# Kernel tuning notes

Measured on AMD Instinct MI355X. Metric: run time of the kernel, lower is better.

## Reference

```python
import jax, jax.numpy as jnp
import numpy as np

EPS = 1e-5

def _ln(x, g, b):
    mu = jnp.mean(x, axis=-1, keepdims=True)
    var = jnp.mean((x - mu) ** 2, axis=-1, keepdims=True)
    return (x - mu) * jax.lax.rsqrt(var + EPS) * g + b

def setup_inputs() -> dict:
    key = jax.random.key(0)
    ks = jax.random.split(key, 12)
    B, T, D, H = 8, 2048, 64, 8
    hs = D // H  # 8
    s = 0.05
    return {
        'x': jax.random.normal(ks[0], (B, T, D), dtype=jnp.float32),
        # per-head Q/K/V weights stacked: [H, hs, D] (torch Linear weight layout [out, in])
        'Wq': jax.random.normal(ks[1], (H, hs, D), dtype=jnp.float32) * s,
        'Wk': jax.random.normal(ks[2], (H, hs, D), dtype=jnp.float32) * s,
        'Wv': jax.random.normal(ks[3], (H, hs, D), dtype=jnp.float32) * s,
        'Wproj': jax.random.normal(ks[4], (D, H * hs), dtype=jnp.float32) * s,
        'bproj': jnp.zeros((D,), dtype=jnp.float32),
        'W1': jax.random.normal(ks[5], (4 * D, D), dtype=jnp.float32) * s,
        'b1': jnp.zeros((4 * D,), dtype=jnp.float32),
        'W2': jax.random.normal(ks[6], (D, 4 * D), dtype=jnp.float32) * s,
        'b2': jnp.zeros((D,), dtype=jnp.float32),
        'ln1_g': jnp.ones((D,), dtype=jnp.float32),
        'ln1_b': jnp.zeros((D,), dtype=jnp.float32),
        'ln2_g': jnp.ones((D,), dtype=jnp.float32),
        'ln2_b': jnp.zeros((D,), dtype=jnp.float32),
    }

def reference(x, Wq, Wk, Wv, Wproj, bproj, W1, b1, W2, b2, ln1_g, ln1_b, ln2_g, ln2_b):
    # pre-LN self-attention (dropout = identity, eval mode)
    h = _ln(x, ln1_g, ln1_b)
    q = jnp.einsum('btd,hsd->bhts', h, Wq)  # [B,H,T,hs]
    k = jnp.einsum('btd,hsd->bhts', h, Wk)
    v = jnp.einsum('btd,hsd->bhts', h, Wv)
    scale = Wk.shape[1] ** -0.5  # k.shape[-1]**-0.5 in original
    wei = jax.nn.softmax(jnp.einsum('bhts,bhus->bhtu', q, k) * scale, axis=-1)
    o = jnp.einsum('bhtu,bhus->bhts', wei, v)  # [B,H,T,hs]
    B, H, T, hs = o.shape
    o = o.transpose(0, 2, 1, 3).reshape(B, T, H * hs)  # concat heads
    x = x + o @ Wproj.T + bproj
    # pre-LN MLP
    h2 = _ln(x, ln2_g, ln2_b)
    ff = jax.nn.relu(h2 @ W1.T + b1) @ W2.T + b2
    return x + ff
```

## Files before the change

### kernel.cpp

```cpp
#include <hip/hip_runtime.h>
#include <hip/hip_fp16.h>

#define DEV static __device__ __forceinline__

constexpr int NTOK = 8 * 2048;
constexpr float LN_EPS = 1e-5f;

using half4  = __attribute__((ext_vector_type(4))) _Float16;
using half8  = __attribute__((ext_vector_type(8))) _Float16;
using f32x4  = __attribute__((ext_vector_type(4))) float;
using f32x16 = __attribute__((ext_vector_type(16))) float;

DEV __half2 bch2(unsigned u) { return __builtin_bit_cast(__half2, u); }
DEV unsigned bcu(__half2 h)  { return __builtin_bit_cast(unsigned, h); }

#define MFMA16(a, b, c)   __builtin_amdgcn_mfma_f32_16x16x16f16(a, b, c, 0, 0, 0)
#define MFMA32(a, b, c)   __builtin_amdgcn_mfma_f32_32x32x8f16(a, b, c, 0, 0, 0)
#define MFMA32X16(a, b, c) __builtin_amdgcn_mfma_f32_32x32x16_f16(a, b, c, 0, 0, 0)

DEV half4 pk4(float a, float b, float c, float d) {
  unsigned lo = __builtin_bit_cast(unsigned, __builtin_amdgcn_cvt_pkrtz(a, b));
  unsigned hi = __builtin_bit_cast(unsigned, __builtin_amdgcn_cvt_pkrtz(c, d));
  uint2 u = make_uint2(lo, hi);
  return __builtin_bit_cast(half4, u);
}
DEV half8 cat8(uint2 a, uint2 b) {
  uint4 u = make_uint4(a.x, a.y, b.x, b.y);
  return __builtin_bit_cast(half8, u);
}
DEV half8 cat8h(half4 a, half4 b) {
  return cat8(__builtin_bit_cast(uint2, a), __builtin_bit_cast(uint2, b));
}

DEV float schr(float x) {
  return __builtin_bit_cast(float, (int)__builtin_fmaf(x, 8388608.0f, 1064987473.0f));
}

__global__ __launch_bounds__(256) void k_ln_qkv(
    const float* __restrict__ x, const float* __restrict__ Wq,
    const float* __restrict__ Wk, const float* __restrict__ Wv,
    const float* __restrict__ g1, const float* __restrict__ b1g,
    __half* __restrict__ Qo, __half* __restrict__ Ko, __half* __restrict__ Vo)
{
  __shared__ __align__(16) __half WqF[4096];
  __shared__ __align__(16) __half WkF[4096];
  __shared__ __align__(16) __half WvF[4096];
  const int tid = threadIdx.x, lane = tid & 63, wid = tid >> 6;
  const int l15 = lane & 15, gg = lane >> 4;
  const float qs = 0.35355339059327373f * 1.4426950408889634f;
  for (int idx = tid; idx < 1024; idx += 256) {
    int mt = idx >> 8, kt = (idx >> 6) & 3, l = idx & 63;
    int row = l & 15, g = l >> 4;
    int off = (mt * 16 + row) * 64 + kt * 16 + g * 4;
    float4 a = *(const float4*)(Wq + off);
    float4 b = *(const float4*)(Wk + off);
    float4 c = *(const float4*)(Wv + off);
    half4 hq; hq[0] = (_Float16)(a.x*qs); hq[1] = (_Float16)(a.y*qs);
    hq[2] = (_Float16)(a.z*qs); hq[3] = (_Float16)(a.w*qs);
    half4 hk; hk[0] = (_Float16)b.x; hk[1] = (_Float16)b.y;
    hk[2] = (_Float16)b.z; hk[3] = (_Float16)b.w;
    half4 hv; hv[0] = (_Float16)c.x; hv[1] = (_Float16)c.y;
    hv[2] = (_Float16)c.z; hv[3] = (_Float16)c.w;
    *(half4*)&WqF[idx * 4] = hq;
    *(half4*)&WkF[idx * 4] = hk;
    *(half4*)&WvF[idx * 4] = hv;
  }
  __syncthreads();

  const int tok = (blockIdx.x * 4 + wid) * 16 + l15;
  const int b = tok >> 11, t = tok & 2047;
  float4 xv[4];
  float sum = 0.f, sq = 0.f;
  #pragma unroll
  for (int kt = 0; kt < 4; ++kt) {
    xv[kt] = *(const float4*)(x + tok * 64 + kt * 16 + gg * 4);
    sum += xv[kt].x + xv[kt].y + xv[kt].z + xv[kt].w;
    sq  += xv[kt].x*xv[kt].x + xv[kt].y*xv[kt].y
         + xv[kt].z*xv[kt].z + xv[kt].w*xv[kt].w;
  }
  sum += __shfl_xor(sum, 16); sum += __shfl_xor(sum, 32);
  sq  += __shfl_xor(sq, 16);  sq  += __shfl_xor(sq, 32);
  float mu = sum * (1.0f / 64.0f);
  float var = sq * (1.0f / 64.0f) - mu * mu;
  float rs = rsqrtf(var + LN_EPS);
  half4 hb[4];
  #pragma unroll
  for (int kt = 0; kt < 4; ++kt) {
    float4 gv = *(const float4*)(g1 + kt * 16 + gg * 4);
    float4 bv = *(const float4*)(b1g + kt * 16 + gg * 4);
    hb[kt][0] = (_Float16)((xv[kt].x - mu) * rs * gv.x + bv.x);
    hb[kt][1] = (_Float16)((xv[kt].y - mu) * rs * gv.y + bv.y);
    hb[kt][2] = (_Float16)((xv[kt].z - mu) * rs * gv.z + bv.z);
    hb[kt][3] = (_Float16)((xv[kt].w - mu) * rs * gv.w + bv.w);
  }
  const int sbase = gg * 4;
  #pragma unroll
  for (int mt = 0; mt < 4; ++mt) {
    f32x4 oq = {}, ok = {}, ov = {};
    #pragma unroll
    for (int kt = 0; kt < 4; ++kt) {
      half4 q_a = *(const half4*)&WqF[((mt * 4 + kt) * 64 + lane) * 4];
      half4 k_a = *(const half4*)&WkF[((mt * 4 + kt) * 64 + lane) * 4];
      half4 v_a = *(const half4*)&WvF[((mt * 4 + kt) * 64 + lane) * 4];
      oq = MFMA16(q_a, hb[kt], oq);
      ok = MFMA16(k_a, hb[kt], ok);
      ov = MFMA16(v_a, hb[kt], ov);
    }
    const int sg = mt * 16 + sbase;
    const int h = sg >> 3, s = sg & 7;
    const long base = ((long)(b * 8 + h) * 2048 + t) * 8 + s;
    *(half4*)(Qo + base) = pk4(oq[0], oq[1], oq[2], oq[3]);
    *(half4*)(Ko + base) = pk4(ok[0], ok[1], ok[2], ok[3]);
    *(half4*)(Vo + base) = pk4(ov[0], ov[1], ov[2], ov[3]);
  }
}

__global__ __launch_bounds__(256, 4) void k_attn(
    const __half* __restrict__ Qg, const __half* __restrict__ Kg,
    const __half* __restrict__ Vg, __half* __restrict__ Og)
{
  __shared__ __align__(16) char VTs[9 * 4128];
  const int tid = threadIdx.x, lane = tid & 63, wid = tid >> 6;
  const int bh = blockIdx.x;
  const int base = bh << 14;
  const uint4* Vu = (const uint4*)(Vg + base);
  for (int i = tid; i < 1024; i += 256) {
    uint4 a = Vu[2 * i], bq = Vu[2 * i + 1];
    const unsigned short* pa = (const unsigned short*)&a;
    const unsigned short* pb = (const unsigned short*)&bq;
    #pragma unroll
    for (int d = 0; d < 8; ++d) {
      unsigned val = (unsigned)pa[d] | ((unsigned)pb[d] << 16);
      *(unsigned*)(VTs + d * 4128 + i * 4) = val;
    }
    *(unsigned*)(VTs + 8 * 4128 + i * 4) = 0x3C003C00u;
  }
  __syncthreads();

  const int b = bh >> 3, hh = bh & 7;
  const int l31 = lane & 31, hi = lane >> 5;
  const int q0 = blockIdx.y * 128 + wid * 32;
  half4 qf = *(const half4*)((const char*)(Qg + base) + (q0 + l31) * 16 + hi * 8);
  const char* kp = (const char*)(Kg + base) + l31 * 16 + hi * 8;
  const int deff = (l31 <= 8) ? l31 : 8;
  const char* vb = VTs + deff * 4128 + hi * 8;

  const f32x16 z = {};
  f32x16 o0 = {};
  half4 kA[8], kB[8];
  #pragma unroll
  for (int u = 0; u < 8; ++u) kA[u] = *(const half4*)(kp + u * 512);

  #define ATTN_BODY(KF, VB, IMM)                                               \
    {                                                                          \
      f32x16 s0 = MFMA32(KF, qf, z);                                           \
      half4 pa0 = pk4(schr(s0[0]),  schr(s0[1]),  schr(s0[2]),  schr(s0[3]));  \
      half4 pa1 = pk4(schr(s0[4]),  schr(s0[5]),  schr(s0[6]),  schr(s0[7]));  \
      uint2 vl0 = *(const uint2*)((VB) + (IMM));                               \
      uint2 vh0 = *(const uint2*)((VB) + (IMM) + 16);                          \
      o0 = MFMA32X16(cat8(vl0, vh0), cat8h(pa0, pa1), o0);                     \
      half4 pb0 = pk4(schr(s0[8]),  schr(s0[9]),  schr(s0[10]), schr(s0[11])); \
      half4 pb1 = pk4(schr(s0[12]), schr(s0[13]), schr(s0[14]), schr(s0[15])); \
      uint2 vl1 = *(const uint2*)((VB) + (IMM) + 32);                          \
      uint2 vh1 = *(const uint2*)((VB) + (IMM) + 48);                          \
      o0 = MFMA32X16(cat8(vl1, vh1), cat8h(pb0, pb1), o0);                     \
    }

  #pragma unroll 1
  for (int gp = 0; gp < 4; ++gp) {
    const char* vbg = vb + gp * 1024;
    const char* kpe = kp + gp * 8192;
    #pragma unroll
    for (int u = 0; u < 8; ++u) kB[u] = *(const half4*)(kpe + 4096 + u * 512);
    #pragma unroll
    for (int u = 0; u < 8; ++u) ATTN_BODY(kA[u], vbg, u * 64);
    if (gp < 3) {
      #pragma unroll
      for (int u = 0; u < 8; ++u) kA[u] = *(const half4*)(kpe + 8192 + u * 512);
    }
    #pragma unroll
    for (int u = 0; u < 8; ++u) ATTN_BODY(kB[u], vbg, 512 + u * 64);
  }
  #undef ATTN_BODY

  float l0 = __shfl(o0[4], l31);
  float inv = 1.0f / l0;
  half4 r;
  r[0] = (_Float16)(o0[0] * inv); r[1] = (_Float16)(o0[1] * inv);
  r[2] = (_Float16)(o0[2] * inv); r[3] = (_Float16)(o0[3] * inv);
  *(half4*)(Og + ((b * 2048 + q0 + l31) * 64) + hh * 8 + hi * 4) = r;
}

__global__ __launch_bounds__(256) void k_proj_mlp(
    const float* __restrict__ x, const __half* __restrict__ Og,
    const float* __restrict__ Wproj, const float* __restrict__ bproj,
    const float* __restrict__ W1, const float* __restrict__ b1,
    const float* __restrict__ W2, const float* __restrict__ b2,
    const float* __restrict__ g2, const float* __restrict__ bb2,
    float* __restrict__ out)
{
  __shared__ __align__(16) __half WpF[4096];
  __shared__ __align__(16) __half W1F[16384];
  __shared__ __align__(16) __half W2F[16384];
  __shared__ __align__(16) float biasLDS[512];
  const int tid = threadIdx.x, lane = tid & 63, wid = tid >> 6;
  const int l15 = lane & 15, gg = lane >> 4;

  for (int idx = tid; idx < 1024; idx += 256) {
    int mt = idx >> 8, kt = (idx >> 6) & 3, l = idx & 63;
    int row = l & 15, g = l >> 4;
    float4 w = *(const float4*)(Wproj + (mt * 16 + row) * 64 + kt * 16 + g * 4);
    half4 h; h[0] = (_Float16)w.x; h[1] = (_Float16)w.y;
    h[2] = (_Float16)w.z; h[3] = (_Float16)w.w;
    *(half4*)&WpF[idx * 4] = h;
  }
  for (int idx = tid; idx < 4096; idx += 256) {
    int mt2 = idx >> 8, kt = (idx >> 6) & 3, l = idx & 63;
    int row = l & 15, g = l >> 4;
    float4 w = *(const float4*)(W1 + (mt2 * 16 + row) * 64 + kt * 16 + g * 4);
    half4 h; h[0] = (_Float16)w.x; h[1] = (_Float16)w.y;
    h[2] = (_Float16)w.z; h[3] = (_Float16)w.w;
    *(half4*)&W1F[idx * 4] = h;
  }
  for (int idx = tid; idx < 4096; idx += 256) {
    int mt = idx >> 10, kt2 = (idx >> 6) & 15, l = idx & 63;
    int row = l & 15, g = l >> 4;
    float4 w = *(const float4*)(W2 + (mt * 16 + row) * 256 + kt2 * 16 + g * 4);
    half4 h; h[0] = (_Float16)w.x; h[1] = (_Float16)w.y;
    h[2] = (_Float16)w.z; h[3] = (_Float16)w.w;
    *(half4*)&W2F[idx * 4] = h;
  }
  for (int idx = tid; idx < 512; idx += 256) {
    float v;
    if      (idx <  64) v = bproj[idx];
    else if (idx < 128) v = g2[idx - 64];
    else if (idx < 192) v = bb2[idx - 128];
    else if (idx < 256) v = b2[idx - 192];
    else                v = b1[idx - 256];
    biasLDS[idx] = v;
  }
  __syncthreads();

  const int tile = blockIdx.x * 4 + wid;
  const int tok = tile * 16 + l15;

  const __half* orow = Og + tok * 64;
  half4 ob[4];
  #pragma unroll
  for (int kt = 0; kt < 4; ++kt)
    ob[kt] = __builtin_bit_cast(half4, *(const uint2*)(orow + kt * 16 + gg * 4));

  f32x4 acc[4];
  #pragma unroll
  for (int mt = 0; mt < 4; ++mt) {
    float4 xv = *(const float4*)(x + tok * 64 + mt * 16 + gg * 4);
    float4 bp = *(const float4*)&biasLDS[mt * 16 + gg * 4];
    acc[mt] = (f32x4){xv.x + bp.x, xv.y + bp.y, xv.z + bp.z, xv.w + bp.w};
    #pragma unroll
    for (int kt = 0; kt < 4; ++kt) {
      half4 wa = *(const half4*)&WpF[((mt * 4 + kt) * 64 + lane) * 4];
      acc[mt] = MFMA16(wa, ob[kt], acc[mt]);
    }
  }
  float sum = 0.f, sq = 0.f;
  #pragma unroll
  for (int mt = 0; mt < 4; ++mt) {
    #pragma unroll
    for (int r = 0; r < 4; ++r) { float v = acc[mt][r]; sum += v; sq += v * v; }
  }
  sum += __shfl_xor(sum, 16); sum += __shfl_xor(sum, 32);
  sq  += __shfl_xor(sq, 16);  sq  += __shfl_xor(sq, 32);
  float mu = sum * (1.0f / 64.0f);
  float var = sq * (1.0f / 64.0f) - mu * mu;
  float rs = rsqrtf(var + LN_EPS);
  half4 hb[4];
  #pragma unroll
  for (int mt = 0; mt < 4; ++mt) {
    float4 gv = *(const float4*)&biasLDS[64 + mt * 16 + gg * 4];
    float4 bv = *(const float4*)&biasLDS[128 + mt * 16 + gg * 4];
    hb[mt][0] = (_Float16)((acc[mt][0] - mu) * rs * gv.x + bv.x);
    hb[mt][1] = (_Float16)((acc[mt][1] - mu) * rs * gv.y + bv.y);
    hb[mt][2] = (_Float16)((acc[mt][2] - mu) * rs * gv.z + bv.z);
    hb[mt][3] = (_Float16)((acc[mt][3] - mu) * rs * gv.w + bv.w);
  }
  half4 pf[16];
  #pragma unroll
  for (int mt2 = 0; mt2 < 16; ++mt2) {
    float4 b1v = *(const float4*)&biasLDS[256 + mt2 * 16 + gg * 4];
    f32x4 f = (f32x4){b1v.x, b1v.y, b1v.z, b1v.w};
    #pragma unroll
    for (int kt = 0; kt < 4; ++kt) {
      half4 wa = *(const half4*)&W1F[((mt2 * 4 + kt) * 64 + lane) * 4];
      f = MFMA16(wa, hb[kt], f);
    }
    pf[mt2][0] = (_Float16)fmaxf(f[0], 0.f);
    pf[mt2][1] = (_Float16)fmaxf(f[1], 0.f);
    pf[mt2][2] = (_Float16)fmaxf(f[2], 0.f);
    pf[mt2][3] = (_Float16)fmaxf(f[3], 0.f);
  }
  #pragma unroll
  for (int mt = 0; mt < 4; ++mt) {
    float4 b2v = *(const float4*)&biasLDS[192 + mt * 16 + gg * 4];
    f32x4 o = (f32x4){acc[mt][0] + b2v.x, acc[mt][1] + b2v.y,
                      acc[mt][2] + b2v.z, acc[mt][3] + b2v.w};
    #pragma unroll
    for (int kt2 = 0; kt2 < 16; ++kt2) {
      half4 wa = *(const half4*)&W2F[((mt * 16 + kt2) * 64 + lane) * 4];
      o = MFMA16(wa, pf[kt2], o);
    }
    *(float4*)(out + tok * 64 + mt * 16 + gg * 4) =
        make_float4(o[0], o[1], o[2], o[3]);
  }
}

extern "C" void kernel_launch(void* const* d_in, const int* in_sizes, int n_in,
                              void* d_out, int out_size, void* d_ws, size_t ws_size,
                              hipStream_t stream) {
  const float* x     = (const float*)d_in[0];
  const float* Wq    = (const float*)d_in[1];
  const float* Wk    = (const float*)d_in[2];
  const float* Wv    = (const float*)d_in[3];
  const float* Wproj = (const float*)d_in[4];
  const float* bproj = (const float*)d_in[5];
  const float* W1    = (const float*)d_in[6];
  const float* b1    = (const float*)d_in[7];
  const float* W2    = (const float*)d_in[8];
  const float* b2    = (const float*)d_in[9];
  const float* g1    = (const float*)d_in[10];
  const float* bb1   = (const float*)d_in[11];
  const float* g2    = (const float*)d_in[12];
  const float* bb2   = (const float*)d_in[13];
  float* out = (float*)d_out;

  __half* Qh = (__half*)d_ws;
  __half* Kh = Qh + 1048576;
  __half* Vh = Kh + 1048576;
  __half* Oc = Vh + 1048576;

  k_ln_qkv<<<256, 256, 0, stream>>>(x, Wq, Wk, Wv, g1, bb1, Qh, Kh, Vh);
  k_attn<<<dim3(64, 16), 256, 0, stream>>>(Qh, Kh, Vh, Oc);
  k_proj_mlp<<<256, 256, 0, stream>>>(x, Oc, Wproj, bproj, W1, b1, W2, b2,
                                      g2, bb2, out);
}
```

Before: 52.84 us.

## Write V transposed from QKV kernel and stream it directly in attention

The QKV kernel now writes V already transposed into a per-head [9][2048] global buffer, with a ones row for the softmax denominator. This removes the per-block LDS transpose and the __syncthreads from the attention kernel, which was repeated by all 16 query blocks of each head. The attention loop now reads K and transposed V straight from global/L2 with one-step register double buffering and two independent accumulators to break the MFMA dependency chain. The cost is scalar 2-byte scattered stores of V in the first kernel and uncoalesced global loads in place of LDS reads in the hot loop.

Result: slower. 82.40 us (+55.9%).

```diff
diff --git a/kernel.cpp b/kernel.cpp
--- a/kernel.cpp
+++ b/kernel.cpp
@@ -14,8 +14,8 @@
 DEV __half2 bch2(unsigned u) { return __builtin_bit_cast(__half2, u); }
 DEV unsigned bcu(__half2 h)  { return __builtin_bit_cast(unsigned, h); }
 
-#define MFMA16(a, b, c)   __builtin_amdgcn_mfma_f32_16x16x16f16(a, b, c, 0, 0, 0)
-#define MFMA32(a, b, c)   __builtin_amdgcn_mfma_f32_32x32x8f16(a, b, c, 0, 0, 0)
+#define MFMA16(a, b, c)    __builtin_amdgcn_mfma_f32_16x16x16f16(a, b, c, 0, 0, 0)
+#define MFMA32(a, b, c)    __builtin_amdgcn_mfma_f32_32x32x8f16(a, b, c, 0, 0, 0)
 #define MFMA32X16(a, b, c) __builtin_amdgcn_mfma_f32_32x32x16_f16(a, b, c, 0, 0, 0)
 
 DEV half4 pk4(float a, float b, float c, float d) {
@@ -40,7 +40,7 @@
     const float* __restrict__ x, const float* __restrict__ Wq,
     const float* __restrict__ Wk, const float* __restrict__ Wv,
     const float* __restrict__ g1, const float* __restrict__ b1g,
-    __half* __restrict__ Qo, __half* __restrict__ Ko, __half* __restrict__ Vo)
+    __half* __restrict__ Qo, __half* __restrict__ Ko, __half* __restrict__ VTg)
 {
   __shared__ __align__(16) __half WqF[4096];
   __shared__ __align__(16) __half WkF[4096];
@@ -48,6 +48,13 @@
   const int tid = threadIdx.x, lane = tid & 63, wid = tid >> 6;
   const int l15 = lane & 15, gg = lane >> 4;
   const float qs = 0.35355339059327373f * 1.4426950408889634f;
+
+  {
+    int bh_ = blockIdx.x >> 2, qq = blockIdx.x & 3;
+    unsigned* onep = (unsigned*)(VTg + ((bh_ * 9 + 8) * 2048) + qq * 512);
+    onep[tid] = 0x3C003C00u;
+  }
+
   for (int idx = tid; idx < 1024; idx += 256) {
     int mt = idx >> 8, kt = (idx >> 6) & 3, l = idx & 63;
     int row = l & 15, g = l >> 4;
@@ -93,7 +100,6 @@
     hb[kt][2] = (_Float16)((xv[kt].z - mu) * rs * gv.z + bv.z);
     hb[kt][3] = (_Float16)((xv[kt].w - mu) * rs * gv.w + bv.w);
   }
-  const int sbase = gg * 4;
   #pragma unroll
   for (int mt = 0; mt < 4; ++mt) {
     f32x4 oq = {}, ok = {}, ov = {};
@@ -106,88 +112,84 @@
       ok = MFMA16(k_a, hb[kt], ok);
       ov = MFMA16(v_a, hb[kt], ov);
     }
-    const int sg = mt * 16 + sbase;
-    const int h = sg >> 3, s = sg & 7;
-    const long base = ((long)(b * 8 + h) * 2048 + t) * 8 + s;
-    *(half4*)(Qo + base) = pk4(oq[0], oq[1], oq[2], oq[3]);
-    *(half4*)(Ko + base) = pk4(ok[0], ok[1], ok[2], ok[3]);
-    *(half4*)(Vo + base) = pk4(ov[0], ov[1], ov[2], ov[3]);
+    const int sg = mt * 16 + gg * 4;
+    const int h = sg >> 3, sq0 = sg & 7;
+    const long qbase = ((long)(b * 8 + h) * 2048 + t) * 8 + sq0;
+    *(half4*)(Qo + qbase) = pk4(oq[0], oq[1], oq[2], oq[3]);
+    *(half4*)(Ko + qbase) = pk4(ok[0], ok[1], ok[2], ok[3]);
+    __half* vtp = VTg + ((long)((b * 8 + h) * 9 + sq0) * 2048) + t;
+    vtp[0]    = __float2half(ov[0]);
+    vtp[2048] = __float2half(ov[1]);
+    vtp[4096] = __float2half(ov[2]);
+    vtp[6144] = __float2half(ov[3]);
   }
 }
 
 __global__ __launch_bounds__(256, 4) void k_attn(
     const __half* __restrict__ Qg, const __half* __restrict__ Kg,
-    const __half* __restrict__ Vg, __half* __restrict__ Og)
+    const __half* __restrict__ VTg, __half* __restrict__ Og)
 {
-  __shared__ __align__(16) char VTs[9 * 4128];
   const int tid = threadIdx.x, lane = tid & 63, wid = tid >> 6;
   const int bh = blockIdx.x;
   const int base = bh << 14;
-  const uint4* Vu = (const uint4*)(Vg + base);
-  for (int i = tid; i < 1024; i += 256) {
-    uint4 a = Vu[2 * i], bq = Vu[2 * i + 1];
-    const unsigned short* pa = (const unsigned short*)&a;
-    const unsigned short* pb = (const unsigned short*)&bq;
-    #pragma unroll
-    for (int d = 0; d < 8; ++d) {
-      unsigned val = (unsigned)pa[d] | ((unsigned)pb[d] << 16);
-      *(unsigned*)(VTs + d * 4128 + i * 4) = val;
-    }
-    *(unsigned*)(VTs + 8 * 4128 + i * 4) = 0x3C003C00u;
-  }
-  __syncthreads();
-
   const int b = bh >> 3, hh = bh & 7;
   const int l31 = lane & 31, hi = lane >> 5;
   const int q0 = blockIdx.y * 128 + wid * 32;
   half4 qf = *(const half4*)((const char*)(Qg + base) + (q0 + l31) * 16 + hi * 8);
   const char* kp = (const char*)(Kg + base) + l31 * 16 + hi * 8;
   const int deff = (l31 <= 8) ? l31 : 8;
-  const char* vb = VTs + deff * 4128 + hi * 8;
+  const char* vt = (const char*)(VTg + ((bh * 9 + deff) << 11)) + hi * 8;
 
   const f32x16 z = {};
-  f32x16 o0 = {};
-  half4 kA[8], kB[8];
-  #pragma unroll
-  for (int u = 0; u < 8; ++u) kA[u] = *(const half4*)(kp + u * 512);
-
-  #define ATTN_BODY(KF, VB, IMM)                                               \
-    {                                                                          \
-      f32x16 s0 = MFMA32(KF, qf, z);                                           \
-      half4 pa0 = pk4(schr(s0[0]),  schr(s0[1]),  schr(s0[2]),  schr(s0[3]));  \
-      half4 pa1 = pk4(schr(s0[4]),  schr(s0[5]),  schr(s0[6]),  schr(s0[7]));  \
-      uint2 vl0 = *(const uint2*)((VB) + (IMM));                               \
-      uint2 vh0 = *(const uint2*)((VB) + (IMM) + 16);                          \
-      o0 = MFMA32X16(cat8(vl0, vh0), cat8h(pa0, pa1), o0);                     \
-      half4 pb0 = pk4(schr(s0[8]),  schr(s0[9]),  schr(s0[10]), schr(s0[11])); \
-      half4 pb1 = pk4(schr(s0[12]), schr(s0[13]), schr(s0[14]), schr(s0[15])); \
-      uint2 vl1 = *(const uint2*)((VB) + (IMM) + 32);                          \
-      uint2 vh1 = *(const uint2*)((VB) + (IMM) + 48);                          \
-      o0 = MFMA32X16(cat8(vl1, vh1), cat8h(pb0, pb1), o0);                     \
-    }
-
-  #pragma unroll 1
-  for (int gp = 0; gp < 4; ++gp) {
-    const char* vbg = vb + gp * 1024;
-    const char* kpe = kp + gp * 8192;
-    #pragma unroll
-    for (int u = 0; u < 8; ++u) kB[u] = *(const half4*)(kpe + 4096 + u * 512);
-    #pragma unroll
-    for (int u = 0; u < 8; ++u) ATTN_BODY(kA[u], vbg, u * 64);
-    if (gp < 3) {
-      #pragma unroll
-      for (int u = 0; u < 8; ++u) kA[u] = *(const half4*)(kpe + 8192 + u * 512);
-    }
-    #pragma unroll
-    for (int u = 0; u < 8; ++u) ATTN_BODY(kB[u], vbg, 512 + u * 64);
-  }
-  #undef ATTN_BODY
-
-  float l0 = __shfl(o0[4], l31);
+  f32x16 oe = {}, oo = {};
+
+  half4 kfA = *(const half4*)(kp);
+  uint2 aA0 = *(const uint2*)(vt);
+  uint2 aA1 = *(const uint2*)(vt + 16);
+  uint2 aA2 = *(const uint2*)(vt + 32);
+  uint2 aA3 = *(const uint2*)(vt + 48);
+
+  #pragma unroll 4
+  for (int c = 0; c < 64; c += 2) {
+    half4 kfB = *(const half4*)(kp + (c + 1) * 512);
+    uint2 bB0 = *(const uint2*)(vt + (c + 1) * 64);
+    uint2 bB1 = *(const uint2*)(vt + (c + 1) * 64 + 16);
+    uint2 bB2 = *(const uint2*)(vt + (c + 1) * 64 + 32);
+    uint2 bB3 = *(const uint2*)(vt + (c + 1) * 64 + 48);
+    {
+      f32x16 s0 = MFMA32(kfA, qf, z);
+      half4 p0 = pk4(schr(s0[0]),  schr(s0[1]),  schr(s0[2]),  schr(s0[3]));
+      half4 p1 = pk4(schr(s0[4]),  schr(s0[5]),  schr(s0[6]),  schr(s0[7]));
+      oe = MFMA32X16(cat8(aA0, aA1), cat8h(p0, p1), oe);
+      half4 p2 = pk4(schr(s0[8]),  schr(s0[9]),  schr(s0[10]), schr(s0[11]));
+      half4 p3 = pk4(schr(s0[12]), schr(s0[13]), schr(s0[14]), schr(s0[15]));
+      oe = MFMA32X16(cat8(aA2, aA3), cat8h(p2, p3), oe);
+    }
+    if (c < 62) {
+      kfA = *(const half4*)(kp + (c + 2) * 512);
+      aA0 = *(const uint2*)(vt + (c + 2) * 64);
+      aA1 = *(const uint2*)(vt + (c + 2) * 64 + 16);
+      aA2 = *(const uint2*)(vt + (c + 2) * 64 + 32);
+      aA3 = *(const uint2*)(vt + (c + 2) * 64 + 48);
+    }
+    {
+      f32x16 s1 = MFMA32(kfB, qf, z);
+      half4 p0 = pk4(schr(s1[0]),  schr(s1[1]),  schr(s1[2]),  schr(s1[3]));
+      half4 p1 = pk4(schr(s1[4]),  schr(s1[5]),  schr(s1[6]),  schr(s1[7]));
+      oo = MFMA32X16(cat8(bB0, bB1), cat8h(p0, p1), oo);
+      half4 p2 = pk4(schr(s1[8]),  schr(s1[9]),  schr(s1[10]), schr(s1[11]));
+      half4 p3 = pk4(schr(s1[12]), schr(s1[13]), schr(s1[14]), schr(s1[15]));
+      oo = MFMA32X16(cat8(bB2, bB3), cat8h(p2, p3), oo);
+    }
+  }
+
+  float l0 = __shfl(oe[4] + oo[4], l31);
   float inv = 1.0f / l0;
   half4 r;
-  r[0] = (_Float16)(o0[0] * inv); r[1] = (_Float16)(o0[1] * inv);
-  r[2] = (_Float16)(o0[2] * inv); r[3] = (_Float16)(o0[3] * inv);
+  r[0] = (_Float16)((oe[0] + oo[0]) * inv);
+  r[1] = (_Float16)((oe[1] + oo[1]) * inv);
+  r[2] = (_Float16)((oe[2] + oo[2]) * inv);
+  r[3] = (_Float16)((oe[3] + oo[3]) * inv);
   *(half4*)(Og + ((b * 2048 + q0 + l31) * 64) + hh * 8 + hi * 4) = r;
 }
 
@@ -334,11 +336,11 @@
 
   __half* Qh = (__half*)d_ws;
   __half* Kh = Qh + 1048576;
-  __half* Vh = Kh + 1048576;
-  __half* Oc = Vh + 1048576;
-
-  k_ln_qkv<<<256, 256, 0, stream>>>(x, Wq, Wk, Wv, g1, bb1, Qh, Kh, Vh);
-  k_attn<<<dim3(64, 16), 256, 0, stream>>>(Qh, Kh, Vh, Oc);
+  __half* VT = Kh + 1048576;
+  __half* Oc = VT + 64 * 9 * 2048;
+
+  k_ln_qkv<<<256, 256, 0, stream>>>(x, Wq, Wk, Wv, g1, bb1, Qh, Kh, VT);
+  k_attn<<<dim3(64, 16), 256, 0, stream>>>(Qh, Kh, VT, Oc);
   k_proj_mlp<<<256, 256, 0, stream>>>(x, Oc, Wproj, bproj, W1, b1, W2, b2,
                                       g2, bb2, out);
 }
```

## Process two query tiles per wave in attention and loop tiles in MLP kernel

Applied to the files above, without the earlier changes.

Each attention wave now handles 64 queries as two 32-row tiles that share the same K fragments and V loads from LDS, halving the grid in y and the per-query K/V traffic. The proj+MLP kernel launches a quarter as many blocks, and each block loops over four token tiles so the LDS weight staging is amortized. The costs are higher register pressure in attention (two accumulators and two score tiles) and fewer blocks to fill the CUs, which may reduce parallelism on a 256-CU part.

Result: slower. 74.68 us (+41.3%).

```diff
diff --git a/kernel.cpp b/kernel.cpp
--- a/kernel.cpp
+++ b/kernel.cpp
@@ -14,8 +14,8 @@
 DEV __half2 bch2(unsigned u) { return __builtin_bit_cast(__half2, u); }
 DEV unsigned bcu(__half2 h)  { return __builtin_bit_cast(unsigned, h); }
 
-#define MFMA16(a, b, c)   __builtin_amdgcn_mfma_f32_16x16x16f16(a, b, c, 0, 0, 0)
-#define MFMA32(a, b, c)   __builtin_amdgcn_mfma_f32_32x32x8f16(a, b, c, 0, 0, 0)
+#define MFMA16(a, b, c)    __builtin_amdgcn_mfma_f32_16x16x16f16(a, b, c, 0, 0, 0)
+#define MFMA32(a, b, c)    __builtin_amdgcn_mfma_f32_32x32x8f16(a, b, c, 0, 0, 0)
 #define MFMA32X16(a, b, c) __builtin_amdgcn_mfma_f32_32x32x16_f16(a, b, c, 0, 0, 0)
 
 DEV half4 pk4(float a, float b, float c, float d) {
@@ -93,7 +93,6 @@
     hb[kt][2] = (_Float16)((xv[kt].z - mu) * rs * gv.z + bv.z);
     hb[kt][3] = (_Float16)((xv[kt].w - mu) * rs * gv.w + bv.w);
   }
-  const int sbase = gg * 4;
   #pragma unroll
   for (int mt = 0; mt < 4; ++mt) {
     f32x4 oq = {}, ok = {}, ov = {};
@@ -106,7 +105,7 @@
       ok = MFMA16(k_a, hb[kt], ok);
       ov = MFMA16(v_a, hb[kt], ov);
     }
-    const int sg = mt * 16 + sbase;
+    const int sg = mt * 16 + gg * 4;
     const int h = sg >> 3, s = sg & 7;
     const long base = ((long)(b * 8 + h) * 2048 + t) * 8 + s;
     *(half4*)(Qo + base) = pk4(oq[0], oq[1], oq[2], oq[3]);
@@ -139,31 +138,39 @@
 
   const int b = bh >> 3, hh = bh & 7;
   const int l31 = lane & 31, hi = lane >> 5;
-  const int q0 = blockIdx.y * 128 + wid * 32;
-  half4 qf = *(const half4*)((const char*)(Qg + base) + (q0 + l31) * 16 + hi * 8);
+  const int q0 = blockIdx.y * 256 + wid * 64;
+  half4 qf0 = *(const half4*)((const char*)(Qg + base) + (q0 + l31) * 16 + hi * 8);
+  half4 qf1 = *(const half4*)((const char*)(Qg + base) + (q0 + 32 + l31) * 16 + hi * 8);
   const char* kp = (const char*)(Kg + base) + l31 * 16 + hi * 8;
   const int deff = (l31 <= 8) ? l31 : 8;
   const char* vb = VTs + deff * 4128 + hi * 8;
 
   const f32x16 z = {};
-  f32x16 o0 = {};
+  f32x16 o0 = {}, o1 = {};
   half4 kA[8], kB[8];
   #pragma unroll
   for (int u = 0; u < 8; ++u) kA[u] = *(const half4*)(kp + u * 512);
 
   #define ATTN_BODY(KF, VB, IMM)                                               \
     {                                                                          \
-      f32x16 s0 = MFMA32(KF, qf, z);                                           \
+      f32x16 s0 = MFMA32(KF, qf0, z);                                          \
+      f32x16 s1 = MFMA32(KF, qf1, z);                                          \
+      uint2 vl0 = *(const uint2*)((VB) + (IMM));                               \
+      uint2 vh0 = *(const uint2*)((VB) + (IMM) + 16);                          \
+      uint2 vl1 = *(const uint2*)((VB) + (IMM) + 32);                          \
+      uint2 vh1 = *(const uint2*)((VB) + (IMM) + 48);                          \
       half4 pa0 = pk4(schr(s0[0]),  schr(s0[1]),  schr(s0[2]),  schr(s0[3]));  \
       half4 pa1 = pk4(schr(s0[4]),  schr(s0[5]),  schr(s0[6]),  schr(s0[7]));  \
-      uint2 vl0 = *(const uint2*)((VB) + (IMM));                               \
-      uint2 vh0 = *(const uint2*)((VB) + (IMM) + 16);                          \
       o0 = MFMA32X16(cat8(vl0, vh0), cat8h(pa0, pa1), o0);                     \
-      half4 pb0 = pk4(schr(s0[8]),  schr(s0[9]),  schr(s0[10]), schr(s0[11])); \
-      half4 pb1 = pk4(schr(s0[12]), schr(s0[13]), schr(s0[14]), schr(s0[15])); \
-      uint2 vl1 = *(const uint2*)((VB) + (IMM) + 32);                          \
-      uint2 vh1 = *(const uint2*)((VB) + (IMM) + 48);                          \
-      o0 = MFMA32X16(cat8(vl1, vh1), cat8h(pb0, pb1), o0);                     \
+      half4 pb0 = pk4(schr(s1[0]),  schr(s1[1]),  schr(s1[2]),  schr(s1[3]));  \
+      half4 pb1 = pk4(schr(s1[4]),  schr(s1[5]),  schr(s1[6]),  schr(s1[7]));  \
+      o1 = MFMA32X16(cat8(vl0, vh0), cat8h(pb0, pb1), o1);                     \
+      half4 pa2 = pk4(schr(s0[8]),  schr(s0[9]),  schr(s0[10]), schr(s0[11])); \
+      half4 pa3 = pk4(schr(s0[12]), schr(s0[13]), schr(s0[14]), schr(s0[15])); \
+      o0 = MFMA32X16(cat8(vl1, vh1), cat8h(pa2, pa3), o0);                     \
+      half4 pb2 = pk4(schr(s1[8]),  schr(s1[9]),  schr(s1[10]), schr(s1[11])); \
+      half4 pb3 = pk4(schr(s1[12]), schr(s1[13]), schr(s1[14]), schr(s1[15])); \
+      o1 = MFMA32X16(cat8(vl1, vh1), cat8h(pb2, pb3), o1);                     \
     }
 
   #pragma unroll 1
@@ -183,12 +190,22 @@
   }
   #undef ATTN_BODY
 
-  float l0 = __shfl(o0[4], l31);
-  float inv = 1.0f / l0;
-  half4 r;
-  r[0] = (_Float16)(o0[0] * inv); r[1] = (_Float16)(o0[1] * inv);
-  r[2] = (_Float16)(o0[2] * inv); r[3] = (_Float16)(o0[3] * inv);
-  *(half4*)(Og + ((b * 2048 + q0 + l31) * 64) + hh * 8 + hi * 4) = r;
+  {
+    float l0 = __shfl(o0[4], l31);
+    float inv = 1.0f / l0;
+    half4 r;
+    r[0] = (_Float16)(o0[0] * inv); r[1] = (_Float16)(o0[1] * inv);
+    r[2] = (_Float16)(o0[2] * inv); r[3] = (_Float16)(o0[3] * inv);
+    *(half4*)(Og + ((b * 2048 + q0 + l31) * 64) + hh * 8 + hi * 4) = r;
+  }
+  {
+    float l1 = __shfl(o1[4], l31);
+    float inv = 1.0f / l1;
+    half4 r;
+    r[0] = (_Float16)(o1[0] * inv); r[1] = (_Float16)(o1[1] * inv);
+    r[2] = (_Float16)(o1[2] * inv); r[3] = (_Float16)(o1[3] * inv);
+    *(half4*)(Og + ((b * 2048 + q0 + 32 + l31) * 64) + hh * 8 + hi * 4) = r;
+  }
 }
 
 __global__ __launch_bounds__(256) void k_proj_mlp(
@@ -241,75 +258,77 @@
   }
   __syncthreads();
 
-  const int tile = blockIdx.x * 4 + wid;
-  const int tok = tile * 16 + l15;
-
-  const __half* orow = Og + tok * 64;
-  half4 ob[4];
-  #pragma unroll
-  for (int kt = 0; kt < 4; ++kt)
-    ob[kt] = __builtin_bit_cast(half4, *(const uint2*)(orow + kt * 16 + gg * 4));
-
-  f32x4 acc[4];
-  #pragma unroll
-  for (int mt = 0; mt < 4; ++mt) {
-    float4 xv = *(const float4*)(x + tok * 64 + mt * 16 + gg * 4);
-    float4 bp = *(const float4*)&biasLDS[mt * 16 + gg * 4];
-    acc[mt] = (f32x4){xv.x + bp.x, xv.y + bp.y, xv.z + bp.z, xv.w + bp.w};
-    #pragma unroll
-    for (int kt = 0; kt < 4; ++kt) {
-      half4 wa = *(const half4*)&WpF[((mt * 4 + kt) * 64 + lane) * 4];
-      acc[mt] = MFMA16(wa, ob[kt], acc[mt]);
-    }
-  }
-  float sum = 0.f, sq = 0.f;
-  #pragma unroll
-  for (int mt = 0; mt < 4; ++mt) {
-    #pragma unroll
-    for (int r = 0; r < 4; ++r) { float v = acc[mt][r]; sum += v; sq += v * v; }
-  }
-  sum += __shfl_xor(sum, 16); sum += __shfl_xor(sum, 32);
-  sq  += __shfl_xor(sq, 16);  sq  += __shfl_xor(sq, 32);
-  float mu = sum * (1.0f / 64.0f);
-  float var = sq * (1.0f / 64.0f) - mu * mu;
-  float rs = rsqrtf(var + LN_EPS);
-  half4 hb[4];
-  #pragma unroll
-  for (int mt = 0; mt < 4; ++mt) {
-    float4 gv = *(const float4*)&biasLDS[64 + mt * 16 + gg * 4];
-    float4 bv = *(const float4*)&biasLDS[128 + mt * 16 + gg * 4];
-    hb[mt][0] = (_Float16)((acc[mt][0] - mu) * rs * gv.x + bv.x);
-    hb[mt][1] = (_Float16)((acc[mt][1] - mu) * rs * gv.y + bv.y);
-    hb[mt][2] = (_Float16)((acc[mt][2] - mu) * rs * gv.z + bv.z);
-    hb[mt][3] = (_Float16)((acc[mt][3] - mu) * rs * gv.w + bv.w);
-  }
-  half4 pf[16];
-  #pragma unroll
-  for (int mt2 = 0; mt2 < 16; ++mt2) {
-    float4 b1v = *(const float4*)&biasLDS[256 + mt2 * 16 + gg * 4];
-    f32x4 f = (f32x4){b1v.x, b1v.y, b1v.z, b1v.w};
-    #pragma unroll
-    for (int kt = 0; kt < 4; ++kt) {
-      half4 wa = *(const half4*)&W1F[((mt2 * 4 + kt) * 64 + lane) * 4];
-      f = MFMA16(wa, hb[kt], f);
-    }
-    pf[mt2][0] = (_Float16)fmaxf(f[0], 0.f);
-    pf[mt2][1] = (_Float16)fmaxf(f[1], 0.f);
-    pf[mt2][2] = (_Float16)fmaxf(f[2], 0.f);
-    pf[mt2][3] = (_Float16)fmaxf(f[3], 0.f);
-  }
-  #pragma unroll
-  for (int mt = 0; mt < 4; ++mt) {
-    float4 b2v = *(const float4*)&biasLDS[192 + mt * 16 + gg * 4];
-    f32x4 o = (f32x4){acc[mt][0] + b2v.x, acc[mt][1] + b2v.y,
-                      acc[mt][2] + b2v.z, acc[mt][3] + b2v.w};
-    #pragma unroll
-    for (int kt2 = 0; kt2 < 16; ++kt2) {
-      half4 wa = *(const half4*)&W2F[((mt * 16 + kt2) * 64 + lane) * 4];
-      o = MFMA16(wa, pf[kt2], o);
-    }
-    *(float4*)(out + tok * 64 + mt * 16 + gg * 4) =
-        make_float4(o[0], o[1], o[2], o[3]);
+  for (int it = 0; it < 4; ++it) {
+    const int tile = blockIdx.x * 4 + wid + it * 256;
+    const int tok = tile * 16 + l15;
+
+    const __half* orow = Og + tok * 64;
+    half4 ob[4];
+    #pragma unroll
+    for (int kt = 0; kt < 4; ++kt)
+      ob[kt] = __builtin_bit_cast(half4, *(const uint2*)(orow + kt * 16 + gg * 4));
+
+    f32x4 acc[4];
+    #pragma unroll
+    for (int mt = 0; mt < 4; ++mt) {
+      float4 xv = *(const float4*)(x + tok * 64 + mt * 16 + gg * 4);
+      float4 bp = *(const float4*)&biasLDS[mt * 16 + gg * 4];
+      acc[mt] = (f32x4){xv.x + bp.x, xv.y + bp.y, xv.z + bp.z, xv.w + bp.w};
+      #pragma unroll
+      for (int kt = 0; kt < 4; ++kt) {
+        half4 wa = *(const half4*)&WpF[((mt * 4 + kt) * 64 + lane) * 4];
+        acc[mt] = MFMA16(wa, ob[kt], acc[mt]);
+      }
+    }
+    float sum = 0.f, sq = 0.f;
+    #pragma unroll
+    for (int mt = 0; mt < 4; ++mt) {
+      #pragma unroll
+      for (int r = 0; r < 4; ++r) { float v = acc[mt][r]; sum += v; sq += v * v; }
+    }
+    sum += __shfl_xor(sum, 16); sum += __shfl_xor(sum, 32);
+    sq  += __shfl_xor(sq, 16);  sq  += __shfl_xor(sq, 32);
+    float mu = sum * (1.0f / 64.0f);
+    float var = sq * (1.0f / 64.0f) - mu * mu;
+    float rs = rsqrtf(var + LN_EPS);
+    half4 hb[4];
+    #pragma unroll
+    for (int mt = 0; mt < 4; ++mt) {
+      float4 gv = *(const float4*)&biasLDS[64 + mt * 16 + gg * 4];
+      float4 bv = *(const float4*)&biasLDS[128 + mt * 16 + gg * 4];
+      hb[mt][0] = (_Float16)((acc[mt][0] - mu) * rs * gv.x + bv.x);
+      hb[mt][1] = (_Float16)((acc[mt][1] - mu) * rs * gv.y + bv.y);
+      hb[mt][2] = (_Float16)((acc[mt][2] - mu) * rs * gv.z + bv.z);
+      hb[mt][3] = (_Float16)((acc[mt][3] - mu) * rs * gv.w + bv.w);
+    }
+    half4 pf[16];
+    #pragma unroll
+    for (int mt2 = 0; mt2 < 16; ++mt2) {
+      float4 b1v = *(const float4*)&biasLDS[256 + mt2 * 16 + gg * 4];
+      f32x4 f = (f32x4){b1v.x, b1v.y, b1v.z, b1v.w};
+      #pragma unroll
+      for (int kt = 0; kt < 4; ++kt) {
+        half4 wa = *(const half4*)&W1F[((mt2 * 4 + kt) * 64 + lane) * 4];
+        f = MFMA16(wa, hb[kt], f);
+      }
+      pf[mt2][0] = (_Float16)fmaxf(f[0], 0.f);
+      pf[mt2][1] = (_Float16)fmaxf(f[1], 0.f);
+      pf[mt2][2] = (_Float16)fmaxf(f[2], 0.f);
+      pf[mt2][3] = (_Float16)fmaxf(f[3], 0.f);
+    }
+    #pragma unroll
+    for (int mt = 0; mt < 4; ++mt) {
+      float4 b2v = *(const float4*)&biasLDS[192 + mt * 16 + gg * 4];
+      f32x4 o = (f32x4){acc[mt][0] + b2v.x, acc[mt][1] + b2v.y,
+                        acc[mt][2] + b2v.z, acc[mt][3] + b2v.w};
+      #pragma unroll
+      for (int kt2 = 0; kt2 < 16; ++kt2) {
+        half4 wa = *(const half4*)&W2F[((mt * 16 + kt2) * 64 + lane) * 4];
+        o = MFMA16(wa, pf[kt2], o);
+      }
+      *(float4*)(out + tok * 64 + mt * 16 + gg * 4) =
+          make_float4(o[0], o[1], o[2], o[3]);
+    }
   }
 }
 
@@ -338,7 +357,7 @@
   __half* Oc = Vh + 1048576;
 
   k_ln_qkv<<<256, 256, 0, stream>>>(x, Wq, Wk, Wv, g1, bb1, Qh, Kh, Vh);
-  k_attn<<<dim3(64, 16), 256, 0, stream>>>(Qh, Kh, Vh, Oc);
-  k_proj_mlp<<<256, 256, 0, stream>>>(x, Oc, Wproj, bproj, W1, b1, W2, b2,
-                                      g2, bb2, out);
-}
+  k_attn<<<dim3(64, 8), 256, 0, stream>>>(Qh, Kh, Vh, Oc);
+  k_proj_mlp<<<64, 256, 0, stream>>>(x, Oc, Wproj, bproj, W1, b1, W2, b2,
+                                     g2, bb2, out);
+}
```

## Fold Schraudolph exp scaling into Q/K weights and MFMA accumulator bias

Applied to the files above, without the earlier changes.

The Schraudolph exp approximation's multiply-add is removed from the attention inner loop. The 2^23 scale is split across the Q weights (×2048) and K weights (×4096), and the additive bias constant is supplied as the initial MFMA accumulator, so the QK^T MFMA output only needs an int conversion. The QK MFMA for the next key tile is also issued before the PV MFMAs of the current tile, and the PV accumulation is split into two independent accumulators to shorten the dependency chain. The scaled K values stored in fp16 (up to about 4096× the original) risk losing precision or overflowing, and the extra accumulator adds register pressure.

New measurement: 60.07 us. 1.14x slower.

```diff
diff --git a/kernel.cpp b/kernel.cpp
--- a/kernel.cpp
+++ b/kernel.cpp
@@ -14,8 +14,8 @@
 DEV __half2 bch2(unsigned u) { return __builtin_bit_cast(__half2, u); }
 DEV unsigned bcu(__half2 h)  { return __builtin_bit_cast(unsigned, h); }
 
-#define MFMA16(a, b, c)   __builtin_amdgcn_mfma_f32_16x16x16f16(a, b, c, 0, 0, 0)
-#define MFMA32(a, b, c)   __builtin_amdgcn_mfma_f32_32x32x8f16(a, b, c, 0, 0, 0)
+#define MFMA16(a, b, c)    __builtin_amdgcn_mfma_f32_16x16x16f16(a, b, c, 0, 0, 0)
+#define MFMA32(a, b, c)    __builtin_amdgcn_mfma_f32_32x32x8f16(a, b, c, 0, 0, 0)
 #define MFMA32X16(a, b, c) __builtin_amdgcn_mfma_f32_32x32x16_f16(a, b, c, 0, 0, 0)
 
 DEV half4 pk4(float a, float b, float c, float d) {
@@ -31,10 +31,7 @@
 DEV half8 cat8h(half4 a, half4 b) {
   return cat8(__builtin_bit_cast(uint2, a), __builtin_bit_cast(uint2, b));
 }
-
-DEV float schr(float x) {
-  return __builtin_bit_cast(float, (int)__builtin_fmaf(x, 8388608.0f, 1064987473.0f));
-}
+DEV float ib(float x) { return __builtin_bit_cast(float, (int)x); }
 
 __global__ __launch_bounds__(256) void k_ln_qkv(
     const float* __restrict__ x, const float* __restrict__ Wq,
@@ -47,7 +44,8 @@
   __shared__ __align__(16) __half WvF[4096];
   const int tid = threadIdx.x, lane = tid & 63, wid = tid >> 6;
   const int l15 = lane & 15, gg = lane >> 4;
-  const float qs = 0.35355339059327373f * 1.4426950408889634f;
+  const float qs = 0.35355339059327373f * 1.4426950408889634f * 2048.0f;
+  const float ks = 4096.0f;
   for (int idx = tid; idx < 1024; idx += 256) {
     int mt = idx >> 8, kt = (idx >> 6) & 3, l = idx & 63;
     int row = l & 15, g = l >> 4;
@@ -57,8 +55,8 @@
     float4 c = *(const float4*)(Wv + off);
     half4 hq; hq[0] = (_Float16)(a.x*qs); hq[1] = (_Float16)(a.y*qs);
     hq[2] = (_Float16)(a.z*qs); hq[3] = (_Float16)(a.w*qs);
-    half4 hk; hk[0] = (_Float16)b.x; hk[1] = (_Float16)b.y;
-    hk[2] = (_Float16)b.z; hk[3] = (_Float16)b.w;
+    half4 hk; hk[0] = (_Float16)(b.x*ks); hk[1] = (_Float16)(b.y*ks);
+    hk[2] = (_Float16)(b.z*ks); hk[3] = (_Float16)(b.w*ks);
     half4 hv; hv[0] = (_Float16)c.x; hv[1] = (_Float16)c.y;
     hv[2] = (_Float16)c.z; hv[3] = (_Float16)c.w;
     *(half4*)&WqF[idx * 4] = hq;
@@ -93,7 +91,6 @@
     hb[kt][2] = (_Float16)((xv[kt].z - mu) * rs * gv.z + bv.z);
     hb[kt][3] = (_Float16)((xv[kt].w - mu) * rs * gv.w + bv.w);
   }
-  const int sbase = gg * 4;
   #pragma unroll
   for (int mt = 0; mt < 4; ++mt) {
     f32x4 oq = {}, ok = {}, ov = {};
@@ -106,7 +103,7 @@
       ok = MFMA16(k_a, hb[kt], ok);
       ov = MFMA16(v_a, hb[kt], ov);
     }
-    const int sg = mt * 16 + sbase;
+    const int sg = mt * 16 + gg * 4;
     const int h = sg >> 3, s = sg & 7;
     const long base = ((long)(b * 8 + h) * 2048 + t) * 8 + s;
     *(half4*)(Qo + base) = pk4(oq[0], oq[1], oq[2], oq[3]);
@@ -145,26 +142,30 @@
   const int deff = (l31 <= 8) ? l31 : 8;
   const char* vb = VTs + deff * 4128 + hi * 8;
 
-  const f32x16 z = {};
-  f32x16 o0 = {};
+  f32x16 cm;
+  #pragma unroll
+  for (int i = 0; i < 16; ++i) cm[i] = 1064987473.0f;
+
+  f32x16 ol = {}, oh = {};
   half4 kA[8], kB[8];
   #pragma unroll
   for (int u = 0; u < 8; ++u) kA[u] = *(const half4*)(kp + u * 512);
 
-  #define ATTN_BODY(KF, VB, IMM)                                               \
+  #define PVB(SC, VB, IMM)                                                     \
     {                                                                          \
-      f32x16 s0 = MFMA32(KF, qf, z);                                           \
-      half4 pa0 = pk4(schr(s0[0]),  schr(s0[1]),  schr(s0[2]),  schr(s0[3]));  \
-      half4 pa1 = pk4(schr(s0[4]),  schr(s0[5]),  schr(s0[6]),  schr(s0[7]));  \
       uint2 vl0 = *(const uint2*)((VB) + (IMM));                               \
       uint2 vh0 = *(const uint2*)((VB) + (IMM) + 16);                          \
-      o0 = MFMA32X16(cat8(vl0, vh0), cat8h(pa0, pa1), o0);                     \
-      half4 pb0 = pk4(schr(s0[8]),  schr(s0[9]),  schr(s0[10]), schr(s0[11])); \
-      half4 pb1 = pk4(schr(s0[12]), schr(s0[13]), schr(s0[14]), schr(s0[15])); \
       uint2 vl1 = *(const uint2*)((VB) + (IMM) + 32);                          \
       uint2 vh1 = *(const uint2*)((VB) + (IMM) + 48);                          \
-      o0 = MFMA32X16(cat8(vl1, vh1), cat8h(pb0, pb1), o0);                     \
-    }
+      half4 pa0 = pk4(ib(SC[0]),  ib(SC[1]),  ib(SC[2]),  ib(SC[3]));          \
+      half4 pa1 = pk4(ib(SC[4]),  ib(SC[5]),  ib(SC[6]),  ib(SC[7]));          \
+      ol = MFMA32X16(cat8(vl0, vh0), cat8h(pa0, pa1), ol);                     \
+      half4 pa2 = pk4(ib(SC[8]),  ib(SC[9]),  ib(SC[10]), ib(SC[11]));         \
+      half4 pa3 = pk4(ib(SC[12]), ib(SC[13]), ib(SC[14]), ib(SC[15]));         \
+      oh = MFMA32X16(cat8(vl1, vh1), cat8h(pa2, pa3), oh);                     \
+    }
+
+  f32x16 sc = MFMA32(kA[0], qf, cm);
 
   #pragma unroll 1
   for (int gp = 0; gp < 4; ++gp) {
@@ -173,21 +174,32 @@
     #pragma unroll
     for (int u = 0; u < 8; ++u) kB[u] = *(const half4*)(kpe + 4096 + u * 512);
     #pragma unroll
-    for (int u = 0; u < 8; ++u) ATTN_BODY(kA[u], vbg, u * 64);
+    for (int u = 0; u < 8; ++u) {
+      half4 kn = (u < 7) ? kA[u + 1] : kB[0];
+      f32x16 sn = MFMA32(kn, qf, cm);
+      PVB(sc, vbg, u * 64);
+      sc = sn;
+    }
     if (gp < 3) {
       #pragma unroll
       for (int u = 0; u < 8; ++u) kA[u] = *(const half4*)(kpe + 8192 + u * 512);
     }
     #pragma unroll
-    for (int u = 0; u < 8; ++u) ATTN_BODY(kB[u], vbg, 512 + u * 64);
-  }
-  #undef ATTN_BODY
-
-  float l0 = __shfl(o0[4], l31);
+    for (int u = 0; u < 8; ++u) {
+      half4 kn = (u < 7) ? kB[u + 1] : kA[0];
+      f32x16 sn = MFMA32(kn, qf, cm);
+      PVB(sc, vbg, 512 + u * 64);
+      sc = sn;
+    }
+  }
+  #undef PVB
+
+  f32x16 o = ol + oh;
+  float l0 = __shfl(o[4], l31);
   float inv = 1.0f / l0;
   half4 r;
-  r[0] = (_Float16)(o0[0] * inv); r[1] = (_Float16)(o0[1] * inv);
-  r[2] = (_Float16)(o0[2] * inv); r[3] = (_Float16)(o0[3] * inv);
+  r[0] = (_Float16)(o[0] * inv); r[1] = (_Float16)(o[1] * inv);
+  r[2] = (_Float16)(o[2] * inv); r[3] = (_Float16)(o[3] * inv);
   *(half4*)(Og + ((b * 2048 + q0 + l31) * 64) + hh * 8 + hi * 4) = r;
 }
 
```
